# Kernel optimization log

Hardware: AMD Instinct MI355X
Metric: run time of the kernel (lower is better)

The kernel has to match this reference:

```python
import jax, jax.numpy as jnp
import numpy as np

NUM_HEADS = 16


def setup_inputs() -> dict:
    key = jax.random.key(0)
    ks = jax.random.split(key, 9)
    B, S, D = 2, 2048, 2048
    s = 1.0 / np.sqrt(D)
    return {
        "x": jax.random.normal(ks[0], (B, S, D), jnp.float32),
        "Wq": jax.random.normal(ks[1], (D, D), jnp.float32) * s,
        "bq": jax.random.normal(ks[2], (D,), jnp.float32) * 0.01,
        "Wk": jax.random.normal(ks[3], (D, D), jnp.float32) * s,
        "bk": jax.random.normal(ks[4], (D,), jnp.float32) * 0.01,
        "Wv": jax.random.normal(ks[5], (D, D), jnp.float32) * s,
        "bv": jax.random.normal(ks[6], (D,), jnp.float32) * 0.01,
        "Wo": jax.random.normal(ks[7], (D, D), jnp.float32) * s,
        "bo": jax.random.normal(ks[8], (D,), jnp.float32) * 0.01,
    }


def reference(x, Wq, bq, Wk, bk, Wv, bv, Wo, bo):
    B, S, D = x.shape
    H = NUM_HEADS
    dh = D // H
    # torch Linear: y = x @ W.T + b
    def proj(W, b):
        return (x @ W.T + b).reshape(B, S, H, dh).transpose(0, 2, 1, 3)  # [B,H,S,dh]
    Q = proj(Wq, bq)
    K = proj(Wk, bk)
    V = proj(Wv, bv)
    scores = jnp.einsum('bhqd,bhkd->bhqk', Q, K) / jnp.sqrt(jnp.float32(dh))
    causal = jnp.tril(jnp.ones((S, S), dtype=bool))  # allow k <= q
    scores = jnp.where(causal, scores, -jnp.inf)
    attn = jax.nn.softmax(scores, axis=-1)
    out = jnp.einsum('bhqk,bhkd->bhqd', attn, V)
    out = out.transpose(0, 2, 1, 3).reshape(B, S, D)
    return out @ Wo.T + bo
```

## Files before the change

kernel.cpp:

```cpp
#include <hip/hip_runtime.h>
#include <hip/hip_bf16.h>

#define B_  2
#define S_  2048
#define D_  2048
#define H_  16
#define DH_ 128
#define M_  (B_*S_)

typedef __hip_bfloat16 bf16;
typedef float v4f __attribute__((ext_vector_type(4)));
typedef short v8s __attribute__((ext_vector_type(8)));

__device__ __forceinline__ short f2s(float x) {
  bf16 h = __float2bfloat16(x);
  return *reinterpret_cast<const short*>(&h);
}
__device__ __forceinline__ v8s ld8(const float* p) {
  v4f a = *reinterpret_cast<const v4f*>(p);
  v4f b = *reinterpret_cast<const v4f*>(p + 4);
  v8s r = { f2s(a[0]), f2s(a[1]), f2s(a[2]), f2s(a[3]),
            f2s(b[0]), f2s(b[1]), f2s(b[2]), f2s(b[3]) };
  return r;
}
__device__ __forceinline__ v8s ld8(const bf16* p) {
  return *reinterpret_cast<const v8s*>(p);
}
__device__ __forceinline__ void store_out(bf16* p, float v)  { *p = __float2bfloat16(v); }
__device__ __forceinline__ void store_out(float* p, float v) { *p = v; }

__device__ __forceinline__ void gll16(const bf16* g, bf16* l) {
  __builtin_amdgcn_global_load_lds((const __attribute__((address_space(1))) void*)g,
                                   (__attribute__((address_space(3))) void*)l,
                                   16, 0, 0);
}

__global__ __launch_bounds__(256) void cvt_f32_bf16(const float* __restrict__ in,
                                                    bf16* __restrict__ out, int n8) {
  int i = blockIdx.x * 256 + threadIdx.x;
  if (i >= n8) return;
  *reinterpret_cast<v8s*>(out + (size_t)i * 8) = ld8(in + (size_t)i * 8);
}

template <int MODE, typename TOUT>
__global__ __launch_bounds__(256) void gemm_bt(const bf16* __restrict__ A,
                                               const bf16* __restrict__ W,
                                               const float* __restrict__ bias,
                                               TOUT* __restrict__ out) {
  __shared__ __align__(16) bf16 As[128 * 32];
  __shared__ __align__(16) bf16 Bs[128 * 32];
  const int tid  = threadIdx.x;
  const int lane = tid & 63, wave = tid >> 6;
  const int wm = wave >> 1, wn = wave & 1;
  const int quad = lane >> 4, l16 = lane & 15;
  const int bm = blockIdx.y * 128, bn = blockIdx.x * 128;

  const bf16* aptr = A + (size_t)(bm + (tid >> 2)) * D_ + (tid & 3) * 8;
  const bf16* bptr = W + (size_t)(bn + (tid >> 2)) * D_ + (tid & 3) * 8;
  bf16* lA0 = As + wave * 512;
  bf16* lA1 = As + 2048 + wave * 512;
  bf16* lB0 = Bs + wave * 512;
  bf16* lB1 = Bs + 2048 + wave * 512;

  v4f acc[4][4] = {};
  for (int k0 = 0; k0 < D_; k0 += 32) {
    gll16(aptr + k0,                    lA0);
    gll16(aptr + (size_t)64 * D_ + k0,  lA1);
    gll16(bptr + k0,                    lB0);
    gll16(bptr + (size_t)64 * D_ + k0,  lB1);
    __syncthreads();
    v8s af[4], bfr[4];
#pragma unroll
    for (int mi = 0; mi < 4; ++mi)
      af[mi] = *reinterpret_cast<const v8s*>(&As[(wm * 64 + mi * 16 + l16) * 32 + quad * 8]);
#pragma unroll
    for (int ni = 0; ni < 4; ++ni)
      bfr[ni] = *reinterpret_cast<const v8s*>(&Bs[(wn * 64 + ni * 16 + l16) * 32 + quad * 8]);
#pragma unroll
    for (int mi = 0; mi < 4; ++mi)
#pragma unroll
      for (int ni = 0; ni < 4; ++ni)
        acc[mi][ni] = __builtin_amdgcn_mfma_f32_16x16x32_bf16(af[mi], bfr[ni], acc[mi][ni], 0, 0, 0);
    __syncthreads();
  }

  constexpr float QSCALE = 0.12752003912f;
#pragma unroll
  for (int ni = 0; ni < 4; ++ni) {
    const int n = bn + wn * 64 + ni * 16 + l16;
    const float bv = bias[n];
#pragma unroll
    for (int mi = 0; mi < 4; ++mi) {
      const int m0 = bm + wm * 64 + mi * 16 + quad * 4;
#pragma unroll
      for (int r = 0; r < 4; ++r) {
        const int m = m0 + r;
        float v = acc[mi][ni][r] + bv;
        size_t idx;
        if (MODE == 0 || MODE == 1) {
          if (MODE == 0) v *= QSCALE;
          int b = m >> 11, s = m & (S_ - 1);
          int h = n >> 7,  d = n & (DH_ - 1);
          idx = ((size_t)(b * H_ + h) * S_ + s) * DH_ + d;
        } else if (MODE == 2) {
          int b = m >> 11, s = m & (S_ - 1);
          int h = n >> 7,  d = n & (DH_ - 1);
          idx = ((size_t)(b * H_ + h) * DH_ + d) * S_ + s;
        } else {
          idx = (size_t)m * D_ + n;
        }
        store_out(out + idx, v);
      }
    }
  }
}

#define QBLK 128
__global__ __launch_bounds__(512, 4) void attn_fused(const bf16* __restrict__ Q,
                                                     const bf16* __restrict__ K,
                                                     const bf16* __restrict__ Vt,
                                                     bf16* __restrict__ Oa) {
  __shared__ __align__(16) bf16 Ks[64 * 128];
  __shared__ __align__(16) bf16 Vs[128 * 64];
  __shared__ __align__(16) bf16 Ps[8][16 * 72];
  const int tid  = threadIdx.x;
  const int lane = tid & 63, wave = tid >> 6;
  const int quad = lane >> 4, l16 = lane & 15;
  const int swz  = l16 & 7;
  const int qt = (int)gridDim.x - 1 - (int)blockIdx.x;
  const int bh = blockIdx.y;
  const int b = bh >> 4, h = bh & 15;
  const bf16* Qh = Q  + (size_t)bh * S_ * DH_;
  const bf16* Kh = K  + (size_t)bh * S_ * DH_;
  const bf16* Vh = Vt + (size_t)bh * DH_ * S_;

  const int qrow0 = qt * QBLK + wave * 16;
  v8s qf[4];
#pragma unroll
  for (int kk = 0; kk < 4; ++kk)
    qf[kk] = *reinterpret_cast<const v8s*>(&Qh[(size_t)(qrow0 + l16) * DH_ + kk * 32 + quad * 8]);

  v4f acc_o[8] = {};
  float m_i[4], l_i[4];
#pragma unroll
  for (int r = 0; r < 4; ++r) { m_i[r] = -1.0e30f; l_i[r] = 0.f; }

  const int nkt = 2 * qt + 2;
  for (int kt = 0; kt < nkt; ++kt) {
    const int kbase = kt * 64;
#pragma unroll
    for (int rr = 0; rr < 2; ++rr) {
      const int g = rr * 512 + tid;
      const int krow = g >> 4, kc = g & 15;
      gll16(Kh + (size_t)(kbase + krow) * DH_ + ((kc ^ (krow & 7)) << 3),
            Ks + rr * 4096 + wave * 512);
      const int vrow = g >> 3, vc = g & 7;
      gll16(Vh + (size_t)vrow * S_ + kbase + ((vc ^ (vrow & 7)) << 3),
            Vs + rr * 4096 + wave * 512);
    }
    __syncthreads();

    const bool active = (kbase <= qrow0 + 15);
    if (active) {
      v4f sc[4];
      __builtin_amdgcn_s_setprio(1);
#pragma unroll
      for (int nt = 0; nt < 4; ++nt) {
        v4f a = {};
#pragma unroll
        for (int kk = 0; kk < 4; ++kk) {
          v8s kf = *reinterpret_cast<const v8s*>(
              &Ks[(nt * 16 + l16) * 128 + (((kk * 4 + quad) ^ swz) << 3)]);
          a = __builtin_amdgcn_mfma_f32_16x16x32_bf16(qf[kk], kf, a, 0, 0, 0);
        }
        sc[nt] = a;
      }
      __builtin_amdgcn_s_setprio(0);
      if (kbase + 63 > qrow0) {
#pragma unroll
        for (int nt = 0; nt < 4; ++nt)
#pragma unroll
          for (int r = 0; r < 4; ++r) {
            int kc2 = kbase + nt * 16 + l16;
            int qr = qrow0 + quad * 4 + r;
            if (kc2 > qr) sc[nt][r] = -1.0e30f;
          }
      }
#pragma unroll
      for (int r = 0; r < 4; ++r) {
        float mx = fmaxf(fmaxf(sc[0][r], sc[1][r]), fmaxf(sc[2][r], sc[3][r]));
        mx = fmaxf(mx, __shfl_xor(mx, 1));
        mx = fmaxf(mx, __shfl_xor(mx, 2));
        mx = fmaxf(mx, __shfl_xor(mx, 4));
        mx = fmaxf(mx, __shfl_xor(mx, 8));
        if (mx > m_i[r] + 8.0f) {
          float alpha = exp2f(m_i[r] - mx);
          m_i[r] = mx;
          l_i[r] *= alpha;
#pragma unroll
          for (int nt8 = 0; nt8 < 8; ++nt8) acc_o[nt8][r] *= alpha;
        }
        const float mm = m_i[r];
        float s0 = exp2f(sc[0][r] - mm);
        float s1 = exp2f(sc[1][r] - mm);
        float s2 = exp2f(sc[2][r] - mm);
        float s3 = exp2f(sc[3][r] - mm);
        sc[0][r] = s0; sc[1][r] = s1; sc[2][r] = s2; sc[3][r] = s3;
        float t = s0 + s1 + s2 + s3;
        t += __shfl_xor(t, 1); t += __shfl_xor(t, 2);
        t += __shfl_xor(t, 4); t += __shfl_xor(t, 8);
        l_i[r] += t;
      }
#pragma unroll
      for (int nt = 0; nt < 4; ++nt)
#pragma unroll
        for (int r = 0; r < 4; ++r)
          Ps[wave][(quad * 4 + r) * 72 + nt * 16 + l16] = __float2bfloat16(sc[nt][r]);
      asm volatile("s_waitcnt lgkmcnt(0)" ::: "memory");
      __builtin_amdgcn_s_setprio(1);
#pragma unroll
      for (int kk2 = 0; kk2 < 2; ++kk2) {
        v8s pf = *reinterpret_cast<const v8s*>(&Ps[wave][l16 * 72 + kk2 * 32 + quad * 8]);
#pragma unroll
        for (int nt8 = 0; nt8 < 8; ++nt8) {
          v8s vf = *reinterpret_cast<const v8s*>(
              &Vs[(nt8 * 16 + l16) * 64 + (((kk2 * 4 + quad) ^ swz) << 3)]);
          acc_o[nt8] = __builtin_amdgcn_mfma_f32_16x16x32_bf16(pf, vf, acc_o[nt8], 0, 0, 0);
        }
      }
      __builtin_amdgcn_s_setprio(0);
    }
    __syncthreads();
  }

#pragma unroll
  for (int r = 0; r < 4; ++r) {
    const float inv = 1.0f / l_i[r];
    const int srow = qrow0 + quad * 4 + r;
#pragma unroll
    for (int nt8 = 0; nt8 < 8; ++nt8)
      Oa[((size_t)b * S_ + srow) * D_ + h * DH_ + nt8 * 16 + l16] =
          __float2bfloat16(acc_o[nt8][r] * inv);
  }
}

extern "C" void kernel_launch(void* const* d_in, const int* in_sizes, int n_in,
                              void* d_out, int out_size, void* d_ws, size_t ws_size,
                              hipStream_t stream) {
  if (n_in != 9 ||
      in_sizes[0] != M_ * D_ ||
      in_sizes[1] != D_ * D_ || in_sizes[2] != D_ ||
      in_sizes[3] != D_ * D_ || in_sizes[4] != D_ ||
      in_sizes[5] != D_ * D_ || in_sizes[6] != D_ ||
      in_sizes[7] != D_ * D_ || in_sizes[8] != D_ ||
      out_size != M_ * D_)
    return;

  const float* x  = (const float*)d_in[0];
  const float* Wq = (const float*)d_in[1];
  const float* bq = (const float*)d_in[2];
  const float* Wk = (const float*)d_in[3];
  const float* bk = (const float*)d_in[4];
  const float* Wv = (const float*)d_in[5];
  const float* bv = (const float*)d_in[6];
  const float* Wo = (const float*)d_in[7];
  const float* bo = (const float*)d_in[8];
  float* out = (float*)d_out;

  const size_t NT = (size_t)M_ * D_;
  bf16* qws   = (bf16*)d_out;
  bf16* xbf   = (bf16*)d_out + NT;
  bf16* kws   = (bf16*)d_ws;
  bf16* vtw   = kws + NT;
  bf16* aws   = vtw + NT;
  bf16* wslot = aws;
  bf16* wo_s  = kws;

  const int N8X = M_ * D_ / 8;
  const int N8W = D_ * D_ / 8;

  dim3 gg(D_ / 128, M_ / 128), bb(256);

  cvt_f32_bf16<<<N8X / 256, bb, 0, stream>>>(x, xbf, N8X);

  cvt_f32_bf16<<<N8W / 256, bb, 0, stream>>>(Wq, wslot, N8W);
  gemm_bt<0, bf16><<<gg, bb, 0, stream>>>(xbf, wslot, bq, qws);

  cvt_f32_bf16<<<N8W / 256, bb, 0, stream>>>(Wk, wslot, N8W);
  gemm_bt<1, bf16><<<gg, bb, 0, stream>>>(xbf, wslot, bk, kws);

  cvt_f32_bf16<<<N8W / 256, bb, 0, stream>>>(Wv, wslot, N8W);
  gemm_bt<2, bf16><<<gg, bb, 0, stream>>>(xbf, wslot, bv, vtw);

  attn_fused<<<dim3(S_ / QBLK, B_ * H_), dim3(512), 0, stream>>>(qws, kws, vtw, aws);

  cvt_f32_bf16<<<N8W / 256, bb, 0, stream>>>(Wo, wo_s, N8W);
  gemm_bt<3, float><<<gg, bb, 0, stream>>>(aws, wo_s, bo, out);
}
```

Baseline: 475.3 us.

## Double-buffer GEMM and attention tiles, fuse Q/K projections into one GEMM

The GEMM is rewritten with 256x128 tiles, a K-step of 64 and double-buffered LDS, so global-to-LDS loads of the next tile overlap the MFMA work on the current one. The Q and K projections become a single launch over a concatenated bf16 weight buffer. The attention kernel also double-buffers its K/V tiles. The aim is to hide memory latency and cut launch count and barrier stalls, at the cost of much more LDS per block (occupancy hint lowered from 4 to 2) and a full vmcnt(0) wait every iteration.

```diff
diff --git a/kernel.cpp b/kernel.cpp
--- a/kernel.cpp
+++ b/kernel.cpp
@@ -23,9 +23,6 @@
             f2s(b[0]), f2s(b[1]), f2s(b[2]), f2s(b[3]) };
   return r;
 }
-__device__ __forceinline__ v8s ld8(const bf16* p) {
-  return *reinterpret_cast<const v8s*>(p);
-}
 __device__ __forceinline__ void store_out(bf16* p, float v)  { *p = __float2bfloat16(v); }
 __device__ __forceinline__ void store_out(float* p, float v) { *p = v; }
 
@@ -43,52 +40,96 @@
 }
 
 template <int MODE, typename TOUT>
-__global__ __launch_bounds__(256) void gemm_bt(const bf16* __restrict__ A,
-                                               const bf16* __restrict__ W,
-                                               const float* __restrict__ bias,
-                                               TOUT* __restrict__ out) {
-  __shared__ __align__(16) bf16 As[128 * 32];
-  __shared__ __align__(16) bf16 Bs[128 * 32];
+__global__ __launch_bounds__(512, 2) void gemm2(const bf16* __restrict__ A,
+                                                const bf16* __restrict__ W,
+                                                const float* __restrict__ bias0,
+                                                const float* __restrict__ bias1,
+                                                TOUT* __restrict__ out0,
+                                                TOUT* __restrict__ out1) {
+  __shared__ __align__(16) bf16 As[2][256 * 64];
+  __shared__ __align__(16) bf16 Bs[2][128 * 64];
   const int tid  = threadIdx.x;
   const int lane = tid & 63, wave = tid >> 6;
   const int wm = wave >> 1, wn = wave & 1;
   const int quad = lane >> 4, l16 = lane & 15;
-  const int bm = blockIdx.y * 128, bn = blockIdx.x * 128;
-
-  const bf16* aptr = A + (size_t)(bm + (tid >> 2)) * D_ + (tid & 3) * 8;
-  const bf16* bptr = W + (size_t)(bn + (tid >> 2)) * D_ + (tid & 3) * 8;
-  bf16* lA0 = As + wave * 512;
-  bf16* lA1 = As + 2048 + wave * 512;
-  bf16* lB0 = Bs + wave * 512;
-  bf16* lB1 = Bs + 2048 + wave * 512;
+  const int bm = blockIdx.y * 256, bn = blockIdx.x * 128;
+
+  const bf16* Arow = A + (size_t)bm * D_;
+  const bf16* Wrow = W + (size_t)bn * D_;
 
   v4f acc[4][4] = {};
-  for (int k0 = 0; k0 < D_; k0 += 32) {
-    gll16(aptr + k0,                    lA0);
-    gll16(aptr + (size_t)64 * D_ + k0,  lA1);
-    gll16(bptr + k0,                    lB0);
-    gll16(bptr + (size_t)64 * D_ + k0,  lB1);
+
+  {
+#pragma unroll
+    for (int j = 0; j < 4; ++j) {
+      const int blk = j * 512 + tid;
+      gll16(Arow + (size_t)(blk >> 3) * D_ + ((blk & 7) << 3),
+            &As[0][(j * 512 + wave * 64) * 8]);
+    }
+#pragma unroll
+    for (int j = 0; j < 2; ++j) {
+      const int blk = j * 512 + tid;
+      gll16(Wrow + (size_t)(blk >> 3) * D_ + ((blk & 7) << 3),
+            &Bs[0][(j * 512 + wave * 64) * 8]);
+    }
+  }
+  asm volatile("s_waitcnt vmcnt(0)" ::: "memory");
+  __syncthreads();
+
+  constexpr int NT = D_ / 64;
+  int cur = 0;
+  for (int t = 0; t < NT; ++t) {
+    if (t + 1 < NT) {
+      const int k0 = (t + 1) * 64;
+      const int nb = cur ^ 1;
+#pragma unroll
+      for (int j = 0; j < 4; ++j) {
+        const int blk = j * 512 + tid;
+        gll16(Arow + (size_t)(blk >> 3) * D_ + k0 + ((blk & 7) << 3),
+              &As[nb][(j * 512 + wave * 64) * 8]);
+      }
+#pragma unroll
+      for (int j = 0; j < 2; ++j) {
+        const int blk = j * 512 + tid;
+        gll16(Wrow + (size_t)(blk >> 3) * D_ + k0 + ((blk & 7) << 3),
+              &Bs[nb][(j * 512 + wave * 64) * 8]);
+      }
+    }
+    v8s af[4][2], bfr[4][2];
+#pragma unroll
+    for (int mi = 0; mi < 4; ++mi)
+#pragma unroll
+      for (int kk = 0; kk < 2; ++kk)
+        af[mi][kk] = *reinterpret_cast<const v8s*>(
+            &As[cur][(wm * 64 + mi * 16 + l16) * 64 + kk * 32 + quad * 8]);
+#pragma unroll
+    for (int ni = 0; ni < 4; ++ni)
+#pragma unroll
+      for (int kk = 0; kk < 2; ++kk)
+        bfr[ni][kk] = *reinterpret_cast<const v8s*>(
+            &Bs[cur][(wn * 64 + ni * 16 + l16) * 64 + kk * 32 + quad * 8]);
+#pragma unroll
+    for (int kk = 0; kk < 2; ++kk)
+#pragma unroll
+      for (int mi = 0; mi < 4; ++mi)
+#pragma unroll
+        for (int ni = 0; ni < 4; ++ni)
+          acc[mi][ni] = __builtin_amdgcn_mfma_f32_16x16x32_bf16(
+              af[mi][kk], bfr[ni][kk], acc[mi][ni], 0, 0, 0);
+    asm volatile("s_waitcnt vmcnt(0)" ::: "memory");
     __syncthreads();
-    v8s af[4], bfr[4];
-#pragma unroll
-    for (int mi = 0; mi < 4; ++mi)
-      af[mi] = *reinterpret_cast<const v8s*>(&As[(wm * 64 + mi * 16 + l16) * 32 + quad * 8]);
-#pragma unroll
-    for (int ni = 0; ni < 4; ++ni)
-      bfr[ni] = *reinterpret_cast<const v8s*>(&Bs[(wn * 64 + ni * 16 + l16) * 32 + quad * 8]);
-#pragma unroll
-    for (int mi = 0; mi < 4; ++mi)
-#pragma unroll
-      for (int ni = 0; ni < 4; ++ni)
-        acc[mi][ni] = __builtin_amdgcn_mfma_f32_16x16x32_bf16(af[mi], bfr[ni], acc[mi][ni], 0, 0, 0);
-    __syncthreads();
+    cur ^= 1;
   }
 
   constexpr float QSCALE = 0.12752003912f;
+  const int proj = (MODE == 0) ? (bn >> 11) : 0;
+  const float* bias = (proj ? bias1 : bias0);
+  TOUT* outp = (proj ? out1 : out0);
+  const int bnl = bn & 2047;
 #pragma unroll
   for (int ni = 0; ni < 4; ++ni) {
-    const int n = bn + wn * 64 + ni * 16 + l16;
-    const float bv = bias[n];
+    const int nl = bnl + wn * 64 + ni * 16 + l16;
+    const float bv = bias[nl];
 #pragma unroll
     for (int mi = 0; mi < 4; ++mi) {
       const int m0 = bm + wm * 64 + mi * 16 + quad * 4;
@@ -97,31 +138,31 @@
         const int m = m0 + r;
         float v = acc[mi][ni][r] + bv;
         size_t idx;
-        if (MODE == 0 || MODE == 1) {
-          if (MODE == 0) v *= QSCALE;
+        if (MODE == 0) {
+          if (!proj) v *= QSCALE;
           int b = m >> 11, s = m & (S_ - 1);
-          int h = n >> 7,  d = n & (DH_ - 1);
+          int h = nl >> 7, d = nl & (DH_ - 1);
           idx = ((size_t)(b * H_ + h) * S_ + s) * DH_ + d;
         } else if (MODE == 2) {
           int b = m >> 11, s = m & (S_ - 1);
-          int h = n >> 7,  d = n & (DH_ - 1);
+          int h = nl >> 7, d = nl & (DH_ - 1);
           idx = ((size_t)(b * H_ + h) * DH_ + d) * S_ + s;
         } else {
-          idx = (size_t)m * D_ + n;
+          idx = (size_t)m * D_ + nl;
         }
-        store_out(out + idx, v);
+        store_out(outp + idx, v);
       }
     }
   }
 }
 
 #define QBLK 128
-__global__ __launch_bounds__(512, 4) void attn_fused(const bf16* __restrict__ Q,
+__global__ __launch_bounds__(512, 2) void attn_fused(const bf16* __restrict__ Q,
                                                      const bf16* __restrict__ K,
                                                      const bf16* __restrict__ Vt,
                                                      bf16* __restrict__ Oa) {
-  __shared__ __align__(16) bf16 Ks[64 * 128];
-  __shared__ __align__(16) bf16 Vs[128 * 64];
+  __shared__ __align__(16) bf16 Ks[2][64 * 128];
+  __shared__ __align__(16) bf16 Vs[2][128 * 64];
   __shared__ __align__(16) bf16 Ps[8][16 * 72];
   const int tid  = threadIdx.x;
   const int lane = tid & 63, wave = tid >> 6;
@@ -146,19 +187,37 @@
   for (int r = 0; r < 4; ++r) { m_i[r] = -1.0e30f; l_i[r] = 0.f; }
 
   const int nkt = 2 * qt + 2;
+
+#pragma unroll
+  for (int rr = 0; rr < 2; ++rr) {
+    const int g = rr * 512 + tid;
+    const int krow = g >> 4, kc = g & 15;
+    gll16(Kh + (size_t)krow * DH_ + (((kc ^ (krow & 7)) << 3)),
+          &Ks[0][(rr * 512 + wave * 64) * 8]);
+    const int vrow = g >> 3, vc = g & 7;
+    gll16(Vh + (size_t)vrow * S_ + ((vc ^ (vrow & 7)) << 3),
+          &Vs[0][(rr * 512 + wave * 64) * 8]);
+  }
+  asm volatile("s_waitcnt vmcnt(0)" ::: "memory");
+  __syncthreads();
+
+  int cur = 0;
   for (int kt = 0; kt < nkt; ++kt) {
     const int kbase = kt * 64;
-#pragma unroll
-    for (int rr = 0; rr < 2; ++rr) {
-      const int g = rr * 512 + tid;
-      const int krow = g >> 4, kc = g & 15;
-      gll16(Kh + (size_t)(kbase + krow) * DH_ + ((kc ^ (krow & 7)) << 3),
-            Ks + rr * 4096 + wave * 512);
-      const int vrow = g >> 3, vc = g & 7;
-      gll16(Vh + (size_t)vrow * S_ + kbase + ((vc ^ (vrow & 7)) << 3),
-            Vs + rr * 4096 + wave * 512);
-    }
-    __syncthreads();
+    if (kt + 1 < nkt) {
+      const int nbase = kbase + 64;
+      const int nb = cur ^ 1;
+#pragma unroll
+      for (int rr = 0; rr < 2; ++rr) {
+        const int g = rr * 512 + tid;
+        const int krow = g >> 4, kc = g & 15;
+        gll16(Kh + (size_t)(nbase + krow) * DH_ + (((kc ^ (krow & 7)) << 3)),
+              &Ks[nb][(rr * 512 + wave * 64) * 8]);
+        const int vrow = g >> 3, vc = g & 7;
+        gll16(Vh + (size_t)vrow * S_ + nbase + (((vc ^ (vrow & 7)) << 3)),
+              &Vs[nb][(rr * 512 + wave * 64) * 8]);
+      }
+    }
 
     const bool active = (kbase <= qrow0 + 15);
     if (active) {
@@ -170,7 +229,7 @@
 #pragma unroll
         for (int kk = 0; kk < 4; ++kk) {
           v8s kf = *reinterpret_cast<const v8s*>(
-              &Ks[(nt * 16 + l16) * 128 + (((kk * 4 + quad) ^ swz) << 3)]);
+              &Ks[cur][(nt * 16 + l16) * 128 + (((kk * 4 + quad) ^ swz) << 3)]);
           a = __builtin_amdgcn_mfma_f32_16x16x32_bf16(qf[kk], kf, a, 0, 0, 0);
         }
         sc[nt] = a;
@@ -224,13 +283,15 @@
 #pragma unroll
         for (int nt8 = 0; nt8 < 8; ++nt8) {
           v8s vf = *reinterpret_cast<const v8s*>(
-              &Vs[(nt8 * 16 + l16) * 64 + (((kk2 * 4 + quad) ^ swz) << 3)]);
+              &Vs[cur][(nt8 * 16 + l16) * 64 + (((kk2 * 4 + quad) ^ swz) << 3)]);
           acc_o[nt8] = __builtin_amdgcn_mfma_f32_16x16x32_bf16(pf, vf, acc_o[nt8], 0, 0, 0);
         }
       }
       __builtin_amdgcn_s_setprio(0);
     }
+    asm volatile("s_waitcnt vmcnt(0)" ::: "memory");
     __syncthreads();
+    cur ^= 1;
   }
 
 #pragma unroll
@@ -268,32 +329,31 @@
   float* out = (float*)d_out;
 
   const size_t NT = (size_t)M_ * D_;
+  const size_t WN = (size_t)D_ * D_;
   bf16* qws   = (bf16*)d_out;
   bf16* xbf   = (bf16*)d_out + NT;
   bf16* kws   = (bf16*)d_ws;
   bf16* vtw   = kws + NT;
   bf16* aws   = vtw + NT;
-  bf16* wslot = aws;
+  bf16* wqk   = aws;
+  bf16* wv_s  = aws;
   bf16* wo_s  = kws;
 
   const int N8X = M_ * D_ / 8;
   const int N8W = D_ * D_ / 8;
 
-  dim3 gg(D_ / 128, M_ / 128), bb(256);
-
+  dim3 bb(256);
   cvt_f32_bf16<<<N8X / 256, bb, 0, stream>>>(x, xbf, N8X);
-
-  cvt_f32_bf16<<<N8W / 256, bb, 0, stream>>>(Wq, wslot, N8W);
-  gemm_bt<0, bf16><<<gg, bb, 0, stream>>>(xbf, wslot, bq, qws);
-
-  cvt_f32_bf16<<<N8W / 256, bb, 0, stream>>>(Wk, wslot, N8W);
-  gemm_bt<1, bf16><<<gg, bb, 0, stream>>>(xbf, wslot, bk, kws);
-
-  cvt_f32_bf16<<<N8W / 256, bb, 0, stream>>>(Wv, wslot, N8W);
-  gemm_bt<2, bf16><<<gg, bb, 0, stream>>>(xbf, wslot, bv, vtw);
+  cvt_f32_bf16<<<N8W / 256, bb, 0, stream>>>(Wq, wqk, N8W);
+  cvt_f32_bf16<<<N8W / 256, bb, 0, stream>>>(Wk, wqk + WN, N8W);
+
+  gemm2<0, bf16><<<dim3(32, 16), dim3(512), 0, stream>>>(xbf, wqk, bq, bk, qws, kws);
+
+  cvt_f32_bf16<<<N8W / 256, bb, 0, stream>>>(Wv, wv_s, N8W);
+  gemm2<2, bf16><<<dim3(16, 16), dim3(512), 0, stream>>>(xbf, wv_s, bv, bv, vtw, vtw);
 
   attn_fused<<<dim3(S_ / QBLK, B_ * H_), dim3(512), 0, stream>>>(qws, kws, vtw, aws);
 
   cvt_f32_bf16<<<N8W / 256, bb, 0, stream>>>(Wo, wo_s, N8W);
-  gemm_bt<3, float><<<gg, bb, 0, stream>>>(aws, wo_s, bo, out);
-}
+  gemm2<3, float><<<dim3(16, 16), dim3(512), 0, stream>>>(aws, wo_s, bo, bo, out, out);
+}
```

After: 599.0 us. +26.0%, slower.
